# Kernel tuning notes

Hardware: AMD Instinct MI355X
Metric: run time of the kernel (lower is better)

Reference implementation:

```python
import jax, jax.numpy as jnp
import numpy as np

P_THRESH = 20  # p=0.2 * 100
# direction -> (di, dj): masked pixel (i,j) writes input[i,j] to x[i+di, j+dj], then avg to x[i,j]
OFFSETS = {0: (-1, -1), 1: (-1, 0), 2: (-1, 1), 3: (0, -1), 4: (0, 0), 5: (0, 1), 6: (1, -1), 7: (1, 0)}


def _shift(a, di, dj):
    """out[i+di, j+dj] = a[i, j] on last two axes; out-of-range -> 0/False."""
    H, W = a.shape[-2], a.shape[-1]
    pad = [(0, 0)] * (a.ndim - 2) + [(max(di, 0), max(-di, 0)), (max(dj, 0), max(-dj, 0))]
    p = jnp.pad(a, pad)
    sh, sw = max(-di, 0), max(-dj, 0)
    return p[..., sh:sh + H, sw:sw + W]


def _avg3x3_reflect(x):
    H, W = x.shape[-2], x.shape[-1]
    p = jnp.pad(x, [(0, 0), (0, 0), (1, 1), (1, 1)], mode='reflect')
    s = jnp.zeros_like(x)
    for i in range(3):
        for j in range(3):
            s = s + p[..., i:i + H, j:j + W]
    return s / 9.0


def brown_forward(input, dir, prob):
    avg = _avg3x3_reflect(input)
    pos = prob <= P_THRESH
    x = input
    for d in range(8):  # sequential, matching torch in-place write order
        di, dj = OFFSETS[d]
        m = (dir == d) & pos
        if d == 4:
            x = jnp.where(m, avg, x)  # mm: only avg write
        else:
            sm = _shift(m, di, dj)                       # neighbor-target mask
            x = jnp.where(sm, _shift(input, di, dj), x)  # x[i+di,j+dj] = input[i,j]
            mv = _shift(sm, -di, -dj)                    # mask restricted to valid region
            x = jnp.where(mv, avg, x)                    # x[i,j] = avg[i,j]
    return x


def setup_inputs() -> dict:
    key = jax.random.key(0)
    k1, k2, k3 = jax.random.split(key, 3)
    shape = (32, 64, 128, 128)
    return {
        'input': jax.random.normal(k1, shape, dtype=jnp.float32),
        'dir': jax.random.randint(k2, shape, 0, 8, dtype=jnp.int32),
        'prob': jax.random.randint(k3, shape, 1, 100, dtype=jnp.int32),
    }


def reference(input, dir, prob):
    return brown_forward(input, dir, prob)
```

## Files before the change

### kernel.cpp

```cpp
#include <hip/hip_runtime.h>
#include <cstddef>

#define H 128
#define W 128
#define P_THRESH 20

typedef float f4u __attribute__((ext_vector_type(4), aligned(4)));
typedef int   i4u __attribute__((ext_vector_type(4), aligned(4)));
typedef float nf2 __attribute__((ext_vector_type(2)));

__global__ __launch_bounds__(256, 8)
void brown_kernel(const float* __restrict__ inp,
                  const int*  __restrict__ dirp,
                  const int*  __restrict__ prb,
                  float* __restrict__ out)
{
    __shared__ unsigned int s_mk[1 + 6 * 33];

    const int tid   = threadIdx.x;
    const int bid   = blockIdx.x;
    const int slice = bid >> 5;
    const int r0    = (bid & 31) << 2;
    const size_t base = (size_t)slice * (size_t)(H * W);

    const int lane = tid & 63;
    const int row  = tid >> 6;
    const int gi   = r0 + row;
    const int j0   = lane << 1;

    const int cl = (lane == 0) ? 0 : ((lane == 63) ? (W - 4) : (j0 - 1));
    const int rT = (gi == 0) ? 1 : gi - 1;
    const int rB = (gi == H - 1) ? H - 2 : gi + 1;
    const float* ip = inp + base;
    const f4u iT = *(const f4u*)(ip + (size_t)rT * W + cl);
    const f4u iM = *(const f4u*)(ip + (size_t)gi * W + cl);
    const f4u iB = *(const f4u*)(ip + (size_t)rB * W + cl);

    if (tid < 192) {
        const int r6 = tid >> 5;
        const int w  = tid & 31;
        const int gr = r0 + r6 - 1;
        unsigned m;
        if ((unsigned)gr < (unsigned)H) {
            const i4u dv = *(const i4u*)(dirp + base + (size_t)gr * W + 4 * w);
            const i4u pv = *(const i4u*)(prb  + base + (size_t)gr * W + 4 * w);
            const unsigned a = (pv.x <= P_THRESH) ? (unsigned)dv.x : 8u;
            const unsigned b = (pv.y <= P_THRESH) ? (unsigned)dv.y : 8u;
            const unsigned c = (pv.z <= P_THRESH) ? (unsigned)dv.z : 8u;
            const unsigned e = (pv.w <= P_THRESH) ? (unsigned)dv.w : 8u;
            m = a | (b << 8) | (c << 16) | (e << 24);
            if (gr == 0) {
                unsigned mm = 0;
                #pragma unroll
                for (int i2 = 0; i2 < 4; ++i2) {
                    unsigned bb = (m >> (8 * i2)) & 255u;
                    bb = (bb <= 2u) ? 8u : bb;
                    mm |= bb << (8 * i2);
                }
                m = mm;
            } else if (gr == H - 1) {
                unsigned mm = 0;
                #pragma unroll
                for (int i2 = 0; i2 < 4; ++i2) {
                    unsigned bb = (m >> (8 * i2)) & 255u;
                    bb = (bb >= 6u) ? 8u : bb;
                    mm |= bb << (8 * i2);
                }
                m = mm;
            }
            if (w == 0) {
                const unsigned b0 = m & 255u;
                if ((0x49u >> b0) & 1u) m = (m & ~255u) | 8u;
            }
            if (w == 31) {
                const unsigned b3 = m >> 24;
                if ((0x24u >> b3) & 1u) m = (m & 0x00FFFFFFu) | (8u << 24);
            }
        } else {
            m = 0x08080808u;
        }
        s_mk[1 + 33 * r6 + w] = m;
        if (w == 31) s_mk[1 + 33 * r6 + 32] = 0x08080808u;
    } else if (tid == 192) {
        s_mk[0] = 0x08080808u;
    }
    __syncthreads();

    unsigned mrow[3];
    #pragma unroll
    for (int dr = 0; dr < 3; ++dr) {
        const int addr = 132 * (row + dr) + (j0 + 3);
        const unsigned w0 = s_mk[addr >> 2];
        const unsigned w1 = s_mk[(addr >> 2) + 1];
        const int sh = 8 * (addr & 3);
        mrow[dr] = (w0 >> sh) | (w1 << (32 - sh));
    }
    const unsigned mT = mrow[0], mM = mrow[1], mB = mrow[2];

    const bool e0 = (lane == 0), e63 = (lane == 63), eE = e0 | e63;
    float vT[4], vM[4], vB[4];
    {
        vT[0] = eE ? iT.y : iT.x;  vT[1] = e0 ? iT.x : (e63 ? iT.z : iT.y);
        vT[2] = e0 ? iT.y : (e63 ? iT.w : iT.z);  vT[3] = eE ? iT.z : iT.w;
        vM[0] = eE ? iM.y : iM.x;  vM[1] = e0 ? iM.x : (e63 ? iM.z : iM.y);
        vM[2] = e0 ? iM.y : (e63 ? iM.w : iM.z);  vM[3] = eE ? iM.z : iM.w;
        vB[0] = eE ? iB.y : iB.x;  vB[1] = e0 ? iB.x : (e63 ? iB.z : iB.y);
        vB[2] = e0 ? iB.y : (e63 ? iB.w : iB.z);  vB[3] = eE ? iB.z : iB.w;
    }

    float cs[4];
    #pragma unroll
    for (int w = 0; w < 4; ++w) cs[w] = vT[w] + vM[w] + vB[w];

    nf2 res;
    #pragma unroll
    for (int p = 0; p < 2; ++p) {
        const float avg = (cs[p] + cs[p + 1] + cs[p + 2]) * (1.0f / 9.0f);
        const unsigned wT = mT >> (8 * p);
        const unsigned wM = mM >> (8 * p);
        const unsigned wB = mB >> (8 * p);

        float val = vM[p + 1];
        int dl = -1;
        if (((wB >> 16) & 255u) == 0u) { val = vB[p + 2]; dl = 0; }
        if (((wB >>  8) & 255u) == 1u) { val = vB[p + 1]; dl = 1; }
        if (( wB        & 255u) == 2u) { val = vB[p];     dl = 2; }
        if (((wM >> 16) & 255u) == 3u) { val = vM[p + 2]; dl = 3; }
        if (( wM        & 255u) == 5u) { val = vM[p];     dl = 5; }
        if (((wT >> 16) & 255u) == 6u) { val = vT[p + 2]; dl = 6; }
        if (((wT >>  8) & 255u) == 7u) { val = vT[p + 1]; dl = 7; }

        const int msel = (int)((wM >> 8) & 255u);
        if ((msel < 8) & (msel >= dl)) val = avg;
        res[p] = val;
    }
    *(nf2*)(out + base + (size_t)gi * W + j0) = res;
}

extern "C" void kernel_launch(void* const* d_in, const int* in_sizes, int n_in,
                              void* d_out, int out_size, void* d_ws, size_t ws_size,
                              hipStream_t stream) {
    const float* inp  = (const float*)d_in[0];
    const int*   dirp = (const int*)d_in[1];
    const int*   prb  = (const int*)d_in[2];
    float* out = (float*)d_out;

    const int slices = in_sizes[0] / (H * W);
    const int grid = slices * 32;
    brown_kernel<<<grid, 256, 0, stream>>>(inp, dirp, prb, out);
}
```

Baseline: 379.6 us.

## Compute two output rows per wavefront and eight rows per block

Each block now covers 8 rows instead of 4, and each wavefront produces two adjacent output rows. It loads four input rows per thread and shares the middle-row column sums. The mask halo shrinks from 6 staged rows per 4 output rows to 10 per 8, which cuts redundant dir/prob and input halo reads. The cost is half as many blocks, more registers per thread and a two-pass mask staging loop.

Result: no change. 383.0 us (+0.9%).

```diff
diff --git a/kernel.cpp b/kernel.cpp
--- a/kernel.cpp
+++ b/kernel.cpp
@@ -15,126 +15,142 @@
                   const int*  __restrict__ prb,
                   float* __restrict__ out)
 {
-    __shared__ unsigned int s_mk[1 + 6 * 33];
+    __shared__ unsigned int s_mk[331];
 
     const int tid   = threadIdx.x;
     const int bid   = blockIdx.x;
-    const int slice = bid >> 5;
-    const int r0    = (bid & 31) << 2;
+    const int slice = bid >> 4;
+    const int r0    = (bid & 15) << 3;
     const size_t base = (size_t)slice * (size_t)(H * W);
 
     const int lane = tid & 63;
-    const int row  = tid >> 6;
-    const int gi   = r0 + row;
+    const int wid  = tid >> 6;
+    const int pr   = r0 + (wid << 1);
     const int j0   = lane << 1;
 
-    const int cl = (lane == 0) ? 0 : ((lane == 63) ? (W - 4) : (j0 - 1));
-    const int rT = (gi == 0) ? 1 : gi - 1;
-    const int rB = (gi == H - 1) ? H - 2 : gi + 1;
+    const int cl  = (lane == 0) ? 0 : ((lane == 63) ? (W - 4) : (j0 - 1));
+    const int gA  = (pr == 0) ? 1 : (pr - 1);
+    const int gD  = (pr == H - 2) ? (H - 2) : (pr + 2);
     const float* ip = inp + base;
-    const f4u iT = *(const f4u*)(ip + (size_t)rT * W + cl);
-    const f4u iM = *(const f4u*)(ip + (size_t)gi * W + cl);
-    const f4u iB = *(const f4u*)(ip + (size_t)rB * W + cl);
+    const f4u iA = *(const f4u*)(ip + (size_t)gA * W + cl);
+    const f4u iB = *(const f4u*)(ip + (size_t)pr * W + cl);
+    const f4u iC = *(const f4u*)(ip + (size_t)(pr + 1) * W + cl);
+    const f4u iD = *(const f4u*)(ip + (size_t)gD * W + cl);
 
-    if (tid < 192) {
-        const int r6 = tid >> 5;
-        const int w  = tid & 31;
-        const int gr = r0 + r6 - 1;
-        unsigned m;
-        if ((unsigned)gr < (unsigned)H) {
-            const i4u dv = *(const i4u*)(dirp + base + (size_t)gr * W + 4 * w);
-            const i4u pv = *(const i4u*)(prb  + base + (size_t)gr * W + 4 * w);
-            const unsigned a = (pv.x <= P_THRESH) ? (unsigned)dv.x : 8u;
-            const unsigned b = (pv.y <= P_THRESH) ? (unsigned)dv.y : 8u;
-            const unsigned c = (pv.z <= P_THRESH) ? (unsigned)dv.z : 8u;
-            const unsigned e = (pv.w <= P_THRESH) ? (unsigned)dv.w : 8u;
-            m = a | (b << 8) | (c << 16) | (e << 24);
-            if (gr == 0) {
-                unsigned mm = 0;
-                #pragma unroll
-                for (int i2 = 0; i2 < 4; ++i2) {
-                    unsigned bb = (m >> (8 * i2)) & 255u;
-                    bb = (bb <= 2u) ? 8u : bb;
-                    mm |= bb << (8 * i2);
+    #pragma unroll
+    for (int it = 0; it < 2; ++it) {
+        const int idx = it * 256 + tid;
+        if (idx < 320) {
+            const int lr = idx >> 5;
+            const int w  = idx & 31;
+            const int gr = r0 + lr - 1;
+            unsigned m;
+            if ((unsigned)gr < (unsigned)H) {
+                const i4u dv = *(const i4u*)(dirp + base + (size_t)gr * W + 4 * w);
+                const i4u pv = *(const i4u*)(prb  + base + (size_t)gr * W + 4 * w);
+                const unsigned a = (pv.x <= P_THRESH) ? (unsigned)dv.x : 8u;
+                const unsigned b = (pv.y <= P_THRESH) ? (unsigned)dv.y : 8u;
+                const unsigned c = (pv.z <= P_THRESH) ? (unsigned)dv.z : 8u;
+                const unsigned e = (pv.w <= P_THRESH) ? (unsigned)dv.w : 8u;
+                m = a | (b << 8) | (c << 16) | (e << 24);
+                if (gr == 0) {
+                    unsigned mm = 0;
+                    #pragma unroll
+                    for (int i2 = 0; i2 < 4; ++i2) {
+                        unsigned bb = (m >> (8 * i2)) & 255u;
+                        bb = (bb <= 2u) ? 8u : bb;
+                        mm |= bb << (8 * i2);
+                    }
+                    m = mm;
+                } else if (gr == H - 1) {
+                    unsigned mm = 0;
+                    #pragma unroll
+                    for (int i2 = 0; i2 < 4; ++i2) {
+                        unsigned bb = (m >> (8 * i2)) & 255u;
+                        bb = (bb >= 6u) ? 8u : bb;
+                        mm |= bb << (8 * i2);
+                    }
+                    m = mm;
                 }
-                m = mm;
-            } else if (gr == H - 1) {
-                unsigned mm = 0;
-                #pragma unroll
-                for (int i2 = 0; i2 < 4; ++i2) {
-                    unsigned bb = (m >> (8 * i2)) & 255u;
-                    bb = (bb >= 6u) ? 8u : bb;
-                    mm |= bb << (8 * i2);
+                if (w == 0) {
+                    const unsigned b0 = m & 255u;
+                    if ((0x49u >> b0) & 1u) m = (m & ~255u) | 8u;
                 }
-                m = mm;
+                if (w == 31) {
+                    const unsigned b3 = m >> 24;
+                    if ((0x24u >> b3) & 1u) m = (m & 0x00FFFFFFu) | (8u << 24);
+                }
+            } else {
+                m = 0x08080808u;
             }
-            if (w == 0) {
-                const unsigned b0 = m & 255u;
-                if ((0x49u >> b0) & 1u) m = (m & ~255u) | 8u;
-            }
-            if (w == 31) {
-                const unsigned b3 = m >> 24;
-                if ((0x24u >> b3) & 1u) m = (m & 0x00FFFFFFu) | (8u << 24);
-            }
-        } else {
-            m = 0x08080808u;
+            s_mk[1 + 33 * lr + w] = m;
+            if (w == 31) s_mk[1 + 33 * lr + 32] = 0x08080808u;
         }
-        s_mk[1 + 33 * r6 + w] = m;
-        if (w == 31) s_mk[1 + 33 * r6 + 32] = 0x08080808u;
-    } else if (tid == 192) {
-        s_mk[0] = 0x08080808u;
     }
+    if (tid == 0) s_mk[0] = 0x08080808u;
     __syncthreads();
 
-    unsigned mrow[3];
+    unsigned mr[4];
     #pragma unroll
-    for (int dr = 0; dr < 3; ++dr) {
-        const int addr = 132 * (row + dr) + (j0 + 3);
+    for (int dr = 0; dr < 4; ++dr) {
+        const int lr   = (wid << 1) + dr;
+        const int addr = 132 * lr + (j0 + 3);
         const unsigned w0 = s_mk[addr >> 2];
         const unsigned w1 = s_mk[(addr >> 2) + 1];
         const int sh = 8 * (addr & 3);
-        mrow[dr] = (w0 >> sh) | (w1 << (32 - sh));
+        mr[dr] = (w0 >> sh) | (w1 << (32 - sh));
     }
-    const unsigned mT = mrow[0], mM = mrow[1], mB = mrow[2];
 
     const bool e0 = (lane == 0), e63 = (lane == 63), eE = e0 | e63;
-    float vT[4], vM[4], vB[4];
-    {
-        vT[0] = eE ? iT.y : iT.x;  vT[1] = e0 ? iT.x : (e63 ? iT.z : iT.y);
-        vT[2] = e0 ? iT.y : (e63 ? iT.w : iT.z);  vT[3] = eE ? iT.z : iT.w;
-        vM[0] = eE ? iM.y : iM.x;  vM[1] = e0 ? iM.x : (e63 ? iM.z : iM.y);
-        vM[2] = e0 ? iM.y : (e63 ? iM.w : iM.z);  vM[3] = eE ? iM.z : iM.w;
-        vB[0] = eE ? iB.y : iB.x;  vB[1] = e0 ? iB.x : (e63 ? iB.z : iB.y);
-        vB[2] = e0 ? iB.y : (e63 ? iB.w : iB.z);  vB[3] = eE ? iB.z : iB.w;
+    auto fixrow = [&](f4u i, float v[4]) {
+        v[0] = eE ? i.y : i.x;
+        v[1] = e0 ? i.x : (e63 ? i.z : i.y);
+        v[2] = e0 ? i.y : (e63 ? i.w : i.z);
+        v[3] = eE ? i.z : i.w;
+    };
+    float v0[4], v1[4], v2[4], v3[4];
+    fixrow(iA, v0); fixrow(iB, v1); fixrow(iC, v2); fixrow(iD, v3);
+
+    float s12[4], csT[4], csB[4];
+    #pragma unroll
+    for (int w = 0; w < 4; ++w) {
+        s12[w] = v1[w] + v2[w];
+        csT[w] = v0[w] + s12[w];
+        csB[w] = s12[w] + v3[w];
     }
 
-    float cs[4];
-    #pragma unroll
-    for (int w = 0; w < 4; ++w) cs[w] = vT[w] + vM[w] + vB[w];
+    auto crow = [&](unsigned mT, unsigned mM, unsigned mB,
+                    const float vT[4], const float vM[4], const float vBo[4],
+                    const float cs[4]) -> nf2 {
+        nf2 res;
+        #pragma unroll
+        for (int p = 0; p < 2; ++p) {
+            const float avg = (cs[p] + cs[p + 1] + cs[p + 2]) * (1.0f / 9.0f);
+            const unsigned wT = mT >> (8 * p);
+            const unsigned wM = mM >> (8 * p);
+            const unsigned wB = mB >> (8 * p);
 
-    nf2 res;
-    #pragma unroll
-    for (int p = 0; p < 2; ++p) {
-        const float avg = (cs[p] + cs[p + 1] + cs[p + 2]) * (1.0f / 9.0f);
-        const unsigned wT = mT >> (8 * p);
-        const unsigned wM = mM >> (8 * p);
-        const unsigned wB = mB >> (8 * p);
+            float val = vM[p + 1];
+            int dl = -1;
+            if (((wB >> 16) & 255u) == 0u) { val = vBo[p + 2]; dl = 0; }
+            if (((wB >>  8) & 255u) == 1u) { val = vBo[p + 1]; dl = 1; }
+            if (( wB        & 255u) == 2u) { val = vBo[p];     dl = 2; }
+            if (((wM >> 16) & 255u) == 3u) { val = vM[p + 2];  dl = 3; }
+            if (( wM        & 255u) == 5u) { val = vM[p];      dl = 5; }
+            if (((wT >> 16) & 255u) == 6u) { val = vT[p + 2];  dl = 6; }
+            if (((wT >>  8) & 255u) == 7u) { val = vT[p + 1];  dl = 7; }
 
-        float val = vM[p + 1];
-        int dl = -1;
-        if (((wB >> 16) & 255u) == 0u) { val = vB[p + 2]; dl = 0; }
-        if (((wB >>  8) & 255u) == 1u) { val = vB[p + 1]; dl = 1; }
-        if (( wB        & 255u) == 2u) { val = vB[p];     dl = 2; }
-        if (((wM >> 16) & 255u) == 3u) { val = vM[p + 2]; dl = 3; }
-        if (( wM        & 255u) == 5u) { val = vM[p];     dl = 5; }
-        if (((wT >> 16) & 255u) == 6u) { val = vT[p + 2]; dl = 6; }
-        if (((wT >>  8) & 255u) == 7u) { val = vT[p + 1]; dl = 7; }
+            const int msel = (int)((wM >> 8) & 255u);
+            if ((msel < 8) & (msel >= dl)) val = avg;
+            res[p] = val;
+        }
+        return res;
+    };
 
-        const int msel = (int)((wM >> 8) & 255u);
-        if ((msel < 8) & (msel >= dl)) val = avg;
-        res[p] = val;
-    }
-    *(nf2*)(out + base + (size_t)gi * W + j0) = res;
+    const nf2 resT = crow(mr[0], mr[1], mr[2], v0, v1, v2, csT);
+    const nf2 resB = crow(mr[1], mr[2], mr[3], v1, v2, v3, csB);
+    *(nf2*)(out + base + (size_t)pr * W + j0)       = resT;
+    *(nf2*)(out + base + (size_t)(pr + 1) * W + j0) = resB;
 }
 
 extern "C" void kernel_launch(void* const* d_in, const int* in_sizes, int n_in,
@@ -146,6 +162,6 @@
     float* out = (float*)d_out;
 
     const int slices = in_sizes[0] / (H * W);
-    const int grid = slices * 32;
+    const int grid = slices * 16;
     brown_kernel<<<grid, 256, 0, stream>>>(inp, dirp, prb, out);
 }
```
